# Kernel tuning notes

Measured on AMD Instinct MI355X. Metric: run time of the kernel, lower is better.

The kernel has to match this reference:

```python
import jax, jax.numpy as jnp
import numpy as np

N = 50000          # nodes (ogbn-products-like subgraph)
E = 800000         # directed edges (avg degree 16)
F_IN, HID, HEADS, OUT = 100, 32, 4, 47
W1 = HID * HEADS   # 128
NEG_SLOPE = 0.2
BN_EPS = 1e-5


def _gatv2(x, src, dst, w_src, w_dst, att, bias, heads, ch):
    """GATv2Conv (PyG semantics, share_weights=False, concat).
    x: [N, F]; src/dst: [Etot] (self-loops already appended);
    w_src/w_dst: [F, heads*ch]; att: [heads, ch]; bias: [heads*ch].
    """
    n = x.shape[0]
    xl = (x @ w_src).reshape(n, heads, ch)   # source-side transform
    xr = (x @ w_dst).reshape(n, heads, ch)   # target-side transform
    # per-edge attention logits: a . leaky_relu(xl[j] + xr[i])  -> [E, heads]
    e = jnp.sum(jax.nn.leaky_relu(xl[src] + xr[dst], NEG_SLOPE) * att, axis=-1)
    # segment softmax over incoming edges of each destination node
    m = jax.ops.segment_max(e, dst, num_segments=n)          # [N, heads]
    ex = jnp.exp(e - m[dst])
    denom = jax.ops.segment_sum(ex, dst, num_segments=n)     # [N, heads]
    alpha = ex / denom[dst]                                  # [E, heads]
    # weighted scatter-add aggregation of source features
    out = jax.ops.segment_sum(alpha[:, :, None] * xl[src], dst, num_segments=n)
    return out.reshape(n, heads * ch) + bias


def _bn_eval(x, g, b, m, v):
    return (x - m) * jax.lax.rsqrt(v + BN_EPS) * g + b


def setup_inputs() -> dict:
    key = jax.random.key(0)
    ks = jax.random.split(key, 32)
    s = 0.1
    inp = {
        "x": jax.random.normal(ks[0], (N, F_IN), jnp.float32),
        "edge_index": jax.random.randint(ks[1], (2, E), 0, N, dtype=jnp.int32),
        "w1_src": jax.random.normal(ks[2], (F_IN, W1), jnp.float32) * s,
        "w1_dst": jax.random.normal(ks[3], (F_IN, W1), jnp.float32) * s,
        "att1": jax.random.normal(ks[4], (HEADS, HID), jnp.float32) * s,
        "b1": jnp.zeros((W1,), jnp.float32),
        "bn1_g": jnp.ones((W1,), jnp.float32),
        "bn1_b": jnp.zeros((W1,), jnp.float32),
        "bn1_m": jax.random.normal(ks[5], (W1,), jnp.float32) * 0.05,
        "bn1_v": jax.random.uniform(ks[6], (W1,), jnp.float32, 0.5, 1.5),
        "res0_w": jax.random.normal(ks[7], (F_IN, W1), jnp.float32) * s,
        "res0_b": jnp.zeros((W1,), jnp.float32),
        "w2_src": jax.random.normal(ks[8], (W1, W1), jnp.float32) * s,
        "w2_dst": jax.random.normal(ks[9], (W1, W1), jnp.float32) * s,
        "att2": jax.random.normal(ks[10], (HEADS, HID), jnp.float32) * s,
        "b2": jnp.zeros((W1,), jnp.float32),
        "bn2_g": jnp.ones((W1,), jnp.float32),
        "bn2_b": jnp.zeros((W1,), jnp.float32),
        "bn2_m": jax.random.normal(ks[11], (W1,), jnp.float32) * 0.05,
        "bn2_v": jax.random.uniform(ks[12], (W1,), jnp.float32, 0.5, 1.5),
        # layer 3: 128 -> 47, heads=1
        "w3_src": jax.random.normal(ks[13], (W1, OUT), jnp.float32) * s,
        "w3_dst": jax.random.normal(ks[14], (W1, OUT), jnp.float32) * s,
        "att3": jax.random.normal(ks[15], (1, OUT), jnp.float32) * s,
        "b3": jnp.zeros((OUT,), jnp.float32),
        "bn3_g": jnp.ones((OUT,), jnp.float32),
        "bn3_b": jnp.zeros((OUT,), jnp.float32),
        "bn3_m": jax.random.normal(ks[16], (OUT,), jnp.float32) * 0.05,
        "bn3_v": jax.random.uniform(ks[17], (OUT,), jnp.float32, 0.5, 1.5),
        "res2_w": jax.random.normal(ks[18], (W1, OUT), jnp.float32) * s,
        "res2_b": jnp.zeros((OUT,), jnp.float32),
    }
    return inp


def reference(x, edge_index,
              w1_src, w1_dst, att1, b1, bn1_g, bn1_b, bn1_m, bn1_v, res0_w, res0_b,
              w2_src, w2_dst, att2, b2, bn2_g, bn2_b, bn2_m, bn2_v,
              w3_src, w3_dst, att3, b3, bn3_g, bn3_b, bn3_m, bn3_v, res2_w, res2_b):
    # add self-loops (PyG GATv2Conv default add_self_loops=True)
    loops = jnp.arange(x.shape[0], dtype=edge_index.dtype)
    src = jnp.concatenate([edge_index[0], loops])
    dst = jnp.concatenate([edge_index[1], loops])

    # layer 1 + linear residual + BN + relu (eval mode: no dropout)
    h = _gatv2(x, src, dst, w1_src, w1_dst, att1, b1, HEADS, HID)
    h = h + (x @ res0_w + res0_b)
    h = jax.nn.relu(_bn_eval(h, bn1_g, bn1_b, bn1_m, bn1_v))

    # layer 2 + identity residual + BN + relu
    h2 = _gatv2(h, src, dst, w2_src, w2_dst, att2, b2, HEADS, HID)
    h2 = h2 + h
    h2 = jax.nn.relu(_bn_eval(h2, bn2_g, bn2_b, bn2_m, bn2_v))

    # layer 3 (heads=1) + linear residual + BN (no relu/dropout on last layer)
    out = _gatv2(h2, src, dst, w3_src, w3_dst, att3, b3, 1, OUT)
    out = out + (h2 @ res2_w + res2_b)
    out = _bn_eval(out, bn3_g, bn3_b, bn3_m, bn3_v)
    return out
```

## Files before the change

kernel.cpp:

```cpp
#include <hip/hip_runtime.h>
#include <math.h>

#define BN_EPS 1e-5f
#define SLOT 96
#define LN16 2.7725887f

typedef _Float16 h2 __attribute__((ext_vector_type(2)));
typedef _Float16 h8 __attribute__((ext_vector_type(8)));
typedef float f2v __attribute__((ext_vector_type(2)));
typedef float float4v __attribute__((ext_vector_type(4)));

static __device__ inline h2 bit_h2(unsigned u) {
    union { unsigned u; h2 h; } c; c.u = u; return c.h;
}
static __device__ inline unsigned bit_u(h2 h) {
    union { unsigned u; h2 h; } c; c.h = h; return c.u;
}

template <int CTRL>
static __device__ inline float dpp_add(float x) {
    int y = __builtin_amdgcn_update_dpp(0, __float_as_int(x), CTRL, 0xF, 0xF, true);
    return x + __int_as_float(y);
}
static __device__ inline float red8_dpp(float t) {
    t = dpp_add<0xB1>(t); t = dpp_add<0x4E>(t); t = dpp_add<0x141>(t);
    return t;
}
static __device__ inline float red16_dpp(float t) {
    t = dpp_add<0xB1>(t); t = dpp_add<0x4E>(t); t = dpp_add<0x141>(t);
    t = dpp_add<0x140>(t);
    return t;
}

static __device__ inline void pack_one(int idx,
                                       const float* p0, const float* p1,
                                       const float* p2,
                                       int w0, int w1, int w2,
                                       int Ksrc, int Ncat,
                                       _Float16* out) {
    int k = idx / Ncat, n = idx - k * Ncat;
    float v = 0.f;
    if (k < Ksrc) {
        if (n < w0) v = p0[(size_t)k * w0 + n];
        else if (n < w0 + w1) v = p1[(size_t)k * w1 + (n - w0)];
        else if (w2 > 0 && n < w0 + w1 + w2) v = p2[(size_t)k * w2 + (n - w0 - w1)];
    }
    int kt = k >> 5, kr = k & 31;
    int quad = kr >> 3, j = kr & 7;
    int nt = n >> 4, nr = n & 15;
    int ntiles = Ncat >> 4;
    out[((size_t)(kt * ntiles + nt) * 64 + quad * 16 + nr) * 8 + j] = (_Float16)v;
}

__global__ __launch_bounds__(256) void prep_scat_k(
    const int* __restrict__ src, const int* __restrict__ dst, int E, int Etot,
    int* __restrict__ cnt, int* __restrict__ esrc, int scatBlocks,
    const float* __restrict__ x, _Float16* __restrict__ A, int N,
    const float* __restrict__ w1s, const float* __restrict__ w1d,
    const float* __restrict__ r0w, const float* __restrict__ w2s,
    const float* __restrict__ w2d, const float* __restrict__ w3s,
    const float* __restrict__ w3d, const float* __restrict__ r2w,
    _Float16* __restrict__ Wb1, _Float16* __restrict__ Wb2,
    _Float16* __restrict__ Wb3) {
    if ((int)blockIdx.x < scatBlocks) {
        int i = blockIdx.x * 256 + threadIdx.x;
        if (i < Etot) {
            int d = (i < E) ? dst[i] : (i - E);
            int s = (i < E) ? src[i] : (i - E);
            int pos = atomicAdd(&cnt[d], 1);
            __builtin_nontemporal_store(s << 9, &esrc[(size_t)d * SLOT + pos]);
        }
        return;
    }
    const int S1 = 128 * 384, S2 = 128 * 256, S3 = 128 * 144;
    int convTot = N * 128;
    int idx = (blockIdx.x - scatBlocks) * 256 + threadIdx.x;
    if (idx < convTot) {
        int n = idx >> 7, k = idx & 127;
        A[idx] = (_Float16)(k < 100 ? x[(size_t)n * 100 + k] : 0.f);
        return;
    }
    int p = idx - convTot;
    if (p < S1) pack_one(p, w1s, w1d, r0w, 128, 128, 128, 100, 384, Wb1);
    else if (p < S1 + S2) pack_one(p - S1, w2s, w2d, nullptr, 128, 128, 0, 128, 256, Wb2);
    else if (p < S1 + S2 + S3) pack_one(p - S1 - S2, w3s, w3d, r2w, 47, 47, 47, 128, 144, Wb3);
}

template <int NT>
__global__ __launch_bounds__(256) void mfma_gemm(const _Float16* __restrict__ A,
                                                 const _Float16* __restrict__ Bp,
                                                 _Float16* __restrict__ XLR,
                                                 float* __restrict__ RES,
                                                 int M, int Ncat,
                                                 int ncat_valid, int res_off,
                                                 int bf_remap, int bf_shift,
                                                 int bf_stride, int res_stride) {
    int mt = (blockIdx.x * 256 + threadIdx.x) >> 6;
    int lane = threadIdx.x & 63;
    int mtiles = M >> 4;
    if (mt >= mtiles) return;
    int ngroups = Ncat / (16 * NT);
    int ntiles = Ncat >> 4;
    int quad = lane >> 4;
    int nr = lane & 15;
    int row = mt * 16 + nr;

    h8 a[4];
#pragma unroll
    for (int kt = 0; kt < 4; kt++)
        a[kt] = *(const h8*)(A + (size_t)row * 128 + kt * 32 + quad * 8);

    int rowb = mt * 16 + quad * 4;
    for (int ng = 0; ng < ngroups; ng++) {
        float4v acc[NT];
#pragma unroll
        for (int t = 0; t < NT; t++) acc[t] = (float4v){0.f, 0.f, 0.f, 0.f};
#pragma unroll
        for (int kt = 0; kt < 4; kt++) {
            const _Float16* bbase =
                Bp + ((size_t)(kt * ntiles + ng * NT) * 64 + lane) * 8;
#pragma unroll
            for (int t = 0; t < NT; t++) {
                h8 b = *(const h8*)(bbase + (size_t)t * 512);
                acc[t] = __builtin_amdgcn_mfma_f32_16x16x32_f16(a[kt], b, acc[t], 0, 0, 0);
            }
        }
#pragma unroll
        for (int t = 0; t < NT; t++) {
            int col = (ng * NT + t) * 16 + nr;
            if (col >= ncat_valid) continue;
            if (col < res_off) {
                int bc = (col >= bf_remap) ? col + bf_shift : col;
#pragma unroll
                for (int r = 0; r < 4; r++)
                    XLR[(size_t)(rowb + r) * bf_stride + bc] = (_Float16)acc[t][r];
            } else {
                int rc = col - res_off;
#pragma unroll
                for (int r = 0; r < 4; r++)
                    RES[(size_t)(rowb + r) * res_stride + rc] = acc[t][r];
            }
        }
    }
}

__global__ __launch_bounds__(256) void gat_agg4_fused(
    const int* __restrict__ cnt, const int* __restrict__ esrc,
    const _Float16* __restrict__ xlr, const float* __restrict__ att,
    const float* __restrict__ RES, const float* __restrict__ resB,
    const float* __restrict__ bias,
    const float* __restrict__ g, const float* __restrict__ bb,
    const float* __restrict__ mm, const float* __restrict__ vv,
    _Float16* __restrict__ hbf, int N, int mode) {
    int d = blockIdx.x * 4 + (threadIdx.x >> 6);
    if (d >= N) return;
    int lane = threadIdx.x & 63;
    int half = lane >> 5;
    int gl = lane & 31;
    int c0 = gl * 4;
    const char* xb = (const char*)xlr + c0 * 2;
    const h2 NS = {(_Float16)0.2f, (_Float16)0.2f};

    uint2 xrv = *(const uint2*)(xb + (size_t)d * 512 + 256);
    h2 xr01 = bit_h2(xrv.x), xr23 = bit_h2(xrv.y);
    float4 af = *(const float4*)(att + c0);
    h2 at01 = {(_Float16)af.x, (_Float16)af.y};
    h2 at23 = {(_Float16)af.z, (_Float16)af.w};

    int beg = d * SLOT;
    int end = beg + cnt[d];
    float den = 0.f;
    h2 acc01 = {(_Float16)0.f, (_Float16)0.f};
    h2 acc23 = acc01;
    int j = beg;
    for (; j + 8 <= end; j += 8) {
        uint2 u[4];
#pragma unroll
        for (int q = 0; q < 4; q++) {
            int o = esrc[j + 2 * q + half];
            u[q] = *(const uint2*)(xb + o);
        }
#pragma unroll
        for (int q = 0; q < 4; q++) {
            h2 a01 = bit_h2(u[q].x), a23 = bit_h2(u[q].y);
            h2 v01 = a01 + xr01, v23 = a23 + xr23;
            v01 = __builtin_elementwise_max(v01, v01 * NS);
            v23 = __builtin_elementwise_max(v23, v23 * NS);
            h2 t2 = v01 * at01 + v23 * at23;
            f2v tf = __builtin_convertvector(t2, f2v);
            float t = red8_dpp(tf.x + tf.y);
            float p = __expf(t - LN16);
            den += p;
            h2 P = {(_Float16)p, (_Float16)p};
            acc01 = P * a01 + acc01;
            acc23 = P * a23 + acc23;
        }
    }
    for (; j < end; j += 2) {
        int jj = j + half;
        bool act = jj < end;
        int o = esrc[act ? jj : (end - 1)];
        uint2 u0 = *(const uint2*)(xb + o);
        h2 a01 = bit_h2(u0.x), a23 = bit_h2(u0.y);
        h2 v01 = a01 + xr01, v23 = a23 + xr23;
        v01 = __builtin_elementwise_max(v01, v01 * NS);
        v23 = __builtin_elementwise_max(v23, v23 * NS);
        h2 t2 = v01 * at01 + v23 * at23;
        f2v tf = __builtin_convertvector(t2, f2v);
        float t = red8_dpp(tf.x + tf.y);
        float p = act ? __expf(t - LN16) : 0.f;
        den += p;
        h2 P = {(_Float16)p, (_Float16)p};
        acc01 = P * a01 + acc01;
        acc23 = P * a23 + acc23;
    }
    den += __shfl_xor(den, 32);
    f2v c01 = __builtin_convertvector(acc01, f2v);
    f2v c23 = __builtin_convertvector(acc23, f2v);
    float f0 = c01.x, f1 = c01.y, fA = c23.x, fB = c23.y;
    f0 += __shfl_xor(f0, 32);
    f1 += __shfl_xor(f1, 32);
    fA += __shfl_xor(fA, 32);
    fB += __shfl_xor(fB, 32);

    if (half == 0) {
        float inv = 1.f / den;
        float4 bi = *(const float4*)(bias + c0);
        float o0 = f0 * inv + bi.x;
        float o1 = f1 * inv + bi.y;
        float o2 = fA * inv + bi.z;
        float o3 = fB * inv + bi.w;
        if (mode == 1) {
            float4 r = *(const float4*)(RES + (size_t)d * 128 + c0);
            float4 rb = *(const float4*)(resB + c0);
            o0 += r.x + rb.x; o1 += r.y + rb.y;
            o2 += r.z + rb.z; o3 += r.w + rb.w;
        } else {
            uint2 hv = *(const uint2*)(hbf + (size_t)d * 128 + c0);
            f2v g01 = __builtin_convertvector(bit_h2(hv.x), f2v);
            f2v g23 = __builtin_convertvector(bit_h2(hv.y), f2v);
            o0 += g01.x; o1 += g01.y; o2 += g23.x; o3 += g23.y;
        }
        float4 gm = *(const float4*)(mm + c0);
        float4 gv = *(const float4*)(vv + c0);
        float4 gg = *(const float4*)(g + c0);
        float4 gb = *(const float4*)(bb + c0);
        o0 = fmaxf((o0 - gm.x) * rsqrtf(gv.x + BN_EPS) * gg.x + gb.x, 0.f);
        o1 = fmaxf((o1 - gm.y) * rsqrtf(gv.y + BN_EPS) * gg.y + gb.y, 0.f);
        o2 = fmaxf((o2 - gm.z) * rsqrtf(gv.z + BN_EPS) * gg.z + gb.z, 0.f);
        o3 = fmaxf((o3 - gm.w) * rsqrtf(gv.w + BN_EPS) * gg.w + gb.w, 0.f);
        h2 s01 = {(_Float16)o0, (_Float16)o1};
        h2 s23 = {(_Float16)o2, (_Float16)o3};
        uint2 w;
        w.x = bit_u(s01);
        w.y = bit_u(s23);
        *(uint2*)(hbf + (size_t)d * 128 + c0) = w;
    }
}

__global__ __launch_bounds__(256) void gat_agg1_fused(
    const int* __restrict__ cnt, const int* __restrict__ esrc,
    const _Float16* __restrict__ xlr, const float* __restrict__ att,
    const float* __restrict__ RES, const float* __restrict__ resB,
    const float* __restrict__ bias,
    const float* __restrict__ g, const float* __restrict__ bb,
    const float* __restrict__ mm, const float* __restrict__ vv,
    float* __restrict__ out, int N) {
    int d = blockIdx.x * 4 + (threadIdx.x >> 6);
    if (d >= N) return;
    int lane = threadIdx.x & 63;
    int gl = lane & 15, grp = lane >> 4;
    const char* xb = (const char*)xlr + gl * 8;
    const h2 NS = {(_Float16)0.2f, (_Float16)0.2f};

    uint2 xrv = *(const uint2*)(xb + (size_t)d * 256 + 128);
    h2 xr01 = bit_h2(xrv.x), xr23 = bit_h2(xrv.y);
    float atf[4];
#pragma unroll
    for (int k = 0; k < 4; k++) {
        int c = gl * 4 + k;
        atf[k] = (c < 47) ? att[c] : 0.f;
    }
    h2 at01 = {(_Float16)atf[0], (_Float16)atf[1]};
    h2 at23 = {(_Float16)atf[2], (_Float16)atf[3]};

    int beg = d * SLOT;
    int end = beg + cnt[d];
    float den = 0.f;
    h2 acc01 = {(_Float16)0.f, (_Float16)0.f};
    h2 acc23 = acc01;
    int j = beg + grp;
    for (; j + 4 < end; j += 8) {
        int o0 = esrc[j] >> 1;
        int o1 = esrc[j + 4] >> 1;
        uint2 u0 = *(const uint2*)(xb + o0);
        uint2 u1 = *(const uint2*)(xb + o1);
        h2 a01 = bit_h2(u0.x), a23 = bit_h2(u0.y);
        h2 b01 = bit_h2(u1.x), b23 = bit_h2(u1.y);
        h2 v01 = a01 + xr01, v23 = a23 + xr23;
        h2 w01 = b01 + xr01, w23 = b23 + xr23;
        v01 = __builtin_elementwise_max(v01, v01 * NS);
        v23 = __builtin_elementwise_max(v23, v23 * NS);
        w01 = __builtin_elementwise_max(w01, w01 * NS);
        w23 = __builtin_elementwise_max(w23, w23 * NS);
        h2 t2a = v01 * at01 + v23 * at23;
        h2 t2b = w01 * at01 + w23 * at23;
        f2v ta = __builtin_convertvector(t2a, f2v);
        f2v tb = __builtin_convertvector(t2b, f2v);
        float t0 = red16_dpp(ta.x + ta.y);
        float t1 = red16_dpp(tb.x + tb.y);
        float p0 = __expf(t0 - LN16);
        float p1 = __expf(t1 - LN16);
        den += p0 + p1;
        h2 P0 = {(_Float16)p0, (_Float16)p0};
        h2 P1 = {(_Float16)p1, (_Float16)p1};
        acc01 = P0 * a01 + acc01;
        acc23 = P0 * a23 + acc23;
        acc01 = P1 * b01 + acc01;
        acc23 = P1 * b23 + acc23;
    }
    if (j < end) {
        int o = esrc[j] >> 1;
        uint2 u0 = *(const uint2*)(xb + o);
        h2 a01 = bit_h2(u0.x), a23 = bit_h2(u0.y);
        h2 v01 = a01 + xr01, v23 = a23 + xr23;
        v01 = __builtin_elementwise_max(v01, v01 * NS);
        v23 = __builtin_elementwise_max(v23, v23 * NS);
        h2 t2 = v01 * at01 + v23 * at23;
        f2v tf = __builtin_convertvector(t2, f2v);
        float t = red16_dpp(tf.x + tf.y);
        float p = __expf(t - LN16);
        den += p;
        h2 P = {(_Float16)p, (_Float16)p};
        acc01 = P * a01 + acc01;
        acc23 = P * a23 + acc23;
    }
    den += __shfl_xor(den, 16);
    den += __shfl_xor(den, 32);
    f2v c01 = __builtin_convertvector(acc01, f2v);
    f2v c23 = __builtin_convertvector(acc23, f2v);
    float f[4] = {c01.x, c01.y, c23.x, c23.y};
#pragma unroll
    for (int k = 0; k < 4; k++) {
        f[k] += __shfl_xor(f[k], 16);
        f[k] += __shfl_xor(f[k], 32);
    }
    if (grp == 0 && gl < 12) {
        float inv = 1.f / den;
#pragma unroll
        for (int k = 0; k < 4; k++) {
            int c = gl * 4 + k;
            if (c < 47) {
                float o = f[k] * inv + bias[c] + RES[(size_t)d * 48 + c] + resB[c];
                o = (o - mm[c]) * rsqrtf(vv[c] + BN_EPS) * g[c] + bb[c];
                out[(size_t)d * 47 + c] = o;
            }
        }
    }
}

extern "C" void kernel_launch(void* const* d_in, const int* in_sizes, int n_in,
                              void* d_out, int out_size, void* d_ws, size_t ws_size,
                              hipStream_t stream) {
    const float* x      = (const float*)d_in[0];
    const int*   ei     = (const int*)d_in[1];
    const float* w1_src = (const float*)d_in[2];
    const float* w1_dst = (const float*)d_in[3];
    const float* att1   = (const float*)d_in[4];
    const float* b1     = (const float*)d_in[5];
    const float* bn1_g  = (const float*)d_in[6];
    const float* bn1_b  = (const float*)d_in[7];
    const float* bn1_m  = (const float*)d_in[8];
    const float* bn1_v  = (const float*)d_in[9];
    const float* res0_w = (const float*)d_in[10];
    const float* res0_b = (const float*)d_in[11];
    const float* w2_src = (const float*)d_in[12];
    const float* w2_dst = (const float*)d_in[13];
    const float* att2   = (const float*)d_in[14];
    const float* b2     = (const float*)d_in[15];
    const float* bn2_g  = (const float*)d_in[16];
    const float* bn2_b  = (const float*)d_in[17];
    const float* bn2_m  = (const float*)d_in[18];
    const float* bn2_v  = (const float*)d_in[19];
    const float* w3_src = (const float*)d_in[20];
    const float* w3_dst = (const float*)d_in[21];
    const float* att3   = (const float*)d_in[22];
    const float* b3     = (const float*)d_in[23];
    const float* bn3_g  = (const float*)d_in[24];
    const float* bn3_b  = (const float*)d_in[25];
    const float* bn3_m  = (const float*)d_in[26];
    const float* bn3_v  = (const float*)d_in[27];
    const float* res2_w = (const float*)d_in[28];
    const float* res2_b = (const float*)d_in[29];

    const int F_IN = 100;
    const int KP = 128;
    const int NC1 = 384, NC2 = 256, NC3 = 144;
    int N = in_sizes[0] / F_IN;
    int E = in_sizes[1] / 2;
    int Etot = E + N;
    const int* src = ei;
    const int* dst = ei + E;

    float* ws = (float*)d_ws;
    size_t o = 0;
    _Float16* XLR = (_Float16*)(ws + o); o += (size_t)N * 128;
    float* B_res = ws + o; o += (size_t)N * 128;
    _Float16* A_h = (_Float16*)(ws + o); o += (size_t)N * 64;
    _Float16* Wb1 = (_Float16*)(ws + o); o += (size_t)KP * NC1 / 2;
    _Float16* Wb2 = (_Float16*)(ws + o); o += (size_t)KP * NC2 / 2;
    _Float16* Wb3 = (_Float16*)(ws + o); o += (size_t)KP * NC3 / 2;
    int* I_cnt  = (int*)(ws + o); o += N;
    int* I_esrc = (int*)(ws + o); o += (size_t)N * SLOT + 4;
    (void)ws_size; (void)n_in; (void)out_size;

    int mtiles = (N + 15) / 16;
    int aggGrid = (N + 3) / 4;
    int gemmGrid = (mtiles + 3) / 4;

    hipMemsetAsync(I_cnt, 0, (size_t)N * sizeof(int), stream);

    {
        int sb = (Etot + 255) / 256;
        int prepTot = N * KP + KP * (NC1 + NC2 + NC3);
        int pb = (prepTot + 255) / 256;
        prep_scat_k<<<sb + pb, 256, 0, stream>>>(
            src, dst, E, Etot, I_cnt, I_esrc, sb, x, A_h, N,
            w1_src, w1_dst, res0_w, w2_src, w2_dst, w3_src, w3_dst, res2_w,
            Wb1, Wb2, Wb3);
    }

    mfma_gemm<4><<<gemmGrid, 256, 0, stream>>>(
        A_h, Wb1, XLR, B_res, N, NC1, 384, 256, 384, 0, 256, 128);
    gat_agg4_fused<<<aggGrid, 256, 0, stream>>>(
        I_cnt, I_esrc, XLR, att1, B_res, res0_b, b1,
        bn1_g, bn1_b, bn1_m, bn1_v, A_h, N, 1);

    mfma_gemm<4><<<gemmGrid, 256, 0, stream>>>(
        A_h, Wb2, XLR, B_res, N, NC2, 256, 256, 256, 0, 256, 128);
    gat_agg4_fused<<<aggGrid, 256, 0, stream>>>(
        I_cnt, I_esrc, XLR, att2, nullptr, nullptr, b2,
        bn2_g, bn2_b, bn2_m, bn2_v, A_h, N, 2);

    mfma_gemm<3><<<gemmGrid, 256, 0, stream>>>(
        A_h, Wb3, XLR, B_res, N, NC3, 141, 94, 47, 17, 128, 48);
    gat_agg1_fused<<<aggGrid, 256, 0, stream>>>(
        I_cnt, I_esrc, XLR, att3, B_res, res2_b, b3,
        bn3_g, bn3_b, bn3_m, bn3_v, (float*)d_out, N);
}
```

Measured before the change: 396.0 us.

## Build CSR via bucketed two-pass binning fused into first GEMM launch

Replaces the per-edge global atomic scatter into per-node slots with a two-pass scheme. Edges are first binned into 256-node buckets, using shared-memory histograms and one global atomic per bucket per block. Blocks prepended to the first GEMM launch then scatter each bucket into per-node slots with shared-memory atomics, which also removes the large count memset. The x-to-half conversion is vectorised to float4 loads. The packed edge word limits source ids to 16 bits, and each bucket is capped at a fixed capacity, so larger graphs or skewed degrees would silently drop edges.

Result: faster. 344.8 us (-12.9%).

```diff
diff --git a/kernel.cpp b/kernel.cpp
--- a/kernel.cpp
+++ b/kernel.cpp
@@ -4,8 +4,10 @@
 #define BN_EPS 1e-5f
 #define SLOT 96
 #define LN16 2.7725887f
+#define BCAP 5120
 
 typedef _Float16 h2 __attribute__((ext_vector_type(2)));
+typedef _Float16 h4 __attribute__((ext_vector_type(4)));
 typedef _Float16 h8 __attribute__((ext_vector_type(8)));
 typedef float f2v __attribute__((ext_vector_type(2)));
 typedef float float4v __attribute__((ext_vector_type(4)));
@@ -52,9 +54,9 @@
     out[((size_t)(kt * ntiles + nt) * 64 + quad * 16 + nr) * 8 + j] = (_Float16)v;
 }
 
-__global__ __launch_bounds__(256) void prep_scat_k(
+__global__ __launch_bounds__(256) void prep_bin_k(
     const int* __restrict__ src, const int* __restrict__ dst, int E, int Etot,
-    int* __restrict__ cnt, int* __restrict__ esrc, int scatBlocks,
+    int* __restrict__ gcnt, int* __restrict__ bbuf, int nbA,
     const float* __restrict__ x, _Float16* __restrict__ A, int N,
     const float* __restrict__ w1s, const float* __restrict__ w1d,
     const float* __restrict__ r0w, const float* __restrict__ w2s,
@@ -62,22 +64,41 @@
     const float* __restrict__ w3d, const float* __restrict__ r2w,
     _Float16* __restrict__ Wb1, _Float16* __restrict__ Wb2,
     _Float16* __restrict__ Wb3) {
-    if ((int)blockIdx.x < scatBlocks) {
-        int i = blockIdx.x * 256 + threadIdx.x;
-        if (i < Etot) {
+    if ((int)blockIdx.x < nbA) {
+        __shared__ int hist[256];
+        __shared__ int base[256];
+        int tid = threadIdx.x;
+        hist[tid] = 0;
+        __syncthreads();
+        int per = (Etot + nbA - 1) / nbA;
+        int e0 = blockIdx.x * per;
+        int e1 = min(e0 + per, Etot);
+        for (int i = e0 + tid; i < e1; i += 256) {
+            int d = (i < E) ? dst[i] : (i - E);
+            atomicAdd(&hist[d >> 8], 1);
+        }
+        __syncthreads();
+        int h = hist[tid];
+        if (h) base[tid] = atomicAdd(&gcnt[tid], h);
+        __syncthreads();
+        for (int i = e0 + tid; i < e1; i += 256) {
             int d = (i < E) ? dst[i] : (i - E);
             int s = (i < E) ? src[i] : (i - E);
-            int pos = atomicAdd(&cnt[d], 1);
-            __builtin_nontemporal_store(s << 9, &esrc[(size_t)d * SLOT + pos]);
+            int b = d >> 8;
+            int off = atomicAdd(&base[b], 1);
+            if (off < BCAP) bbuf[(size_t)b * BCAP + off] = ((d & 255) << 16) | s;
         }
         return;
     }
     const int S1 = 128 * 384, S2 = 128 * 256, S3 = 128 * 144;
-    int convTot = N * 128;
-    int idx = (blockIdx.x - scatBlocks) * 256 + threadIdx.x;
+    int convTot = N * 32;
+    int idx = (blockIdx.x - nbA) * 256 + threadIdx.x;
     if (idx < convTot) {
-        int n = idx >> 7, k = idx & 127;
-        A[idx] = (_Float16)(k < 100 ? x[(size_t)n * 100 + k] : 0.f);
+        int n = idx >> 5, t = idx & 31;
+        float4 v = {0.f, 0.f, 0.f, 0.f};
+        if (t < 25) v = *(const float4*)(x + (size_t)n * 100 + t * 4);
+        h4 o = {(_Float16)v.x, (_Float16)v.y, (_Float16)v.z, (_Float16)v.w};
+        *(h4*)(A + (size_t)n * 128 + t * 4) = o;
         return;
     }
     int p = idx - convTot;
@@ -94,8 +115,35 @@
                                                  int M, int Ncat,
                                                  int ncat_valid, int res_off,
                                                  int bf_remap, int bf_shift,
-                                                 int bf_stride, int res_stride) {
-    int mt = (blockIdx.x * 256 + threadIdx.x) >> 6;
+                                                 int bf_stride, int res_stride,
+                                                 const int* __restrict__ gcnt,
+                                                 const int* __restrict__ bbuf,
+                                                 int* __restrict__ esrc,
+                                                 int* __restrict__ cnt,
+                                                 int scatN, int Nn) {
+    __shared__ int lcnt[256];
+    int bid = blockIdx.x;
+    if (bid < scatN) {
+        int tid = threadIdx.x;
+        lcnt[tid] = 0;
+        __syncthreads();
+        int cb = gcnt[bid];
+        if (cb > BCAP) cb = BCAP;
+        const int* bp = bbuf + (size_t)bid * BCAP;
+        int b0 = bid << 8;
+        for (int i = tid; i < cb; i += 256) {
+            int w = bp[i];
+            int dl = (w >> 16) & 255;
+            int s = w & 0xFFFF;
+            int pos = atomicAdd(&lcnt[dl], 1);
+            esrc[(size_t)(b0 + dl) * SLOT + pos] = s << 9;
+        }
+        __syncthreads();
+        int d = b0 + tid;
+        if (d < Nn) cnt[d] = lcnt[tid];
+        return;
+    }
+    int mt = ((bid - scatN) * 256 + threadIdx.x) >> 6;
     int lane = threadIdx.x & 63;
     int mtiles = M >> 4;
     if (mt >= mtiles) return;
@@ -401,6 +449,7 @@
     int Etot = E + N;
     const int* src = ei;
     const int* dst = ei + E;
+    int nbuck = (N + 255) >> 8;
 
     float* ws = (float*)d_ws;
     size_t o = 0;
@@ -412,38 +461,44 @@
     _Float16* Wb3 = (_Float16*)(ws + o); o += (size_t)KP * NC3 / 2;
     int* I_cnt  = (int*)(ws + o); o += N;
     int* I_esrc = (int*)(ws + o); o += (size_t)N * SLOT + 4;
+    int* I_gcnt = (int*)(ws + o); o += 256;
+    int* I_bbuf = (int*)(ws + o); o += (size_t)nbuck * BCAP;
     (void)ws_size; (void)n_in; (void)out_size;
 
     int mtiles = (N + 15) / 16;
     int aggGrid = (N + 3) / 4;
     int gemmGrid = (mtiles + 3) / 4;
 
-    hipMemsetAsync(I_cnt, 0, (size_t)N * sizeof(int), stream);
+    hipMemsetAsync(I_gcnt, 0, 256 * sizeof(int), stream);
 
     {
-        int sb = (Etot + 255) / 256;
-        int prepTot = N * KP + KP * (NC1 + NC2 + NC3);
-        int pb = (prepTot + 255) / 256;
-        prep_scat_k<<<sb + pb, 256, 0, stream>>>(
-            src, dst, E, Etot, I_cnt, I_esrc, sb, x, A_h, N,
+        int nbA = 512;
+        int convTot = N * 32;
+        int packTot = KP * (NC1 + NC2 + NC3);
+        int pb = (convTot + packTot + 255) / 256;
+        prep_bin_k<<<nbA + pb, 256, 0, stream>>>(
+            src, dst, E, Etot, I_gcnt, I_bbuf, nbA, x, A_h, N,
             w1_src, w1_dst, res0_w, w2_src, w2_dst, w3_src, w3_dst, res2_w,
             Wb1, Wb2, Wb3);
     }
 
-    mfma_gemm<4><<<gemmGrid, 256, 0, stream>>>(
-        A_h, Wb1, XLR, B_res, N, NC1, 384, 256, 384, 0, 256, 128);
+    mfma_gemm<4><<<nbuck + gemmGrid, 256, 0, stream>>>(
+        A_h, Wb1, XLR, B_res, N, NC1, 384, 256, 384, 0, 256, 128,
+        I_gcnt, I_bbuf, I_esrc, I_cnt, nbuck, N);
     gat_agg4_fused<<<aggGrid, 256, 0, stream>>>(
         I_cnt, I_esrc, XLR, att1, B_res, res0_b, b1,
         bn1_g, bn1_b, bn1_m, bn1_v, A_h, N, 1);
 
     mfma_gemm<4><<<gemmGrid, 256, 0, stream>>>(
-        A_h, Wb2, XLR, B_res, N, NC2, 256, 256, 256, 0, 256, 128);
+        A_h, Wb2, XLR, B_res, N, NC2, 256, 256, 256, 0, 256, 128,
+        nullptr, nullptr, nullptr, nullptr, 0, N);
     gat_agg4_fused<<<aggGrid, 256, 0, stream>>>(
         I_cnt, I_esrc, XLR, att2, nullptr, nullptr, b2,
         bn2_g, bn2_b, bn2_m, bn2_v, A_h, N, 2);
 
     mfma_gemm<3><<<gemmGrid, 256, 0, stream>>>(
-        A_h, Wb3, XLR, B_res, N, NC3, 141, 94, 47, 17, 128, 48);
+        A_h, Wb3, XLR, B_res, N, NC3, 141, 94, 47, 17, 128, 48,
+        nullptr, nullptr, nullptr, nullptr, 0, N);
     gat_agg1_fused<<<aggGrid, 256, 0, stream>>>(
         I_cnt, I_esrc, XLR, att3, B_res, res2_b, b3,
         bn3_g, bn3_b, bn3_m, bn3_v, (float*)d_out, N);
```
